# Kernel tuning notes

Measured on AMD Instinct MI355X. Metric: run time of the kernel, lower is better.

Reference implementation:

```python
import jax, jax.numpy as jnp
import numpy as np

SHAPE = (4096, 8192)


def setup_inputs() -> dict:
    key = jax.random.key(0)
    k1, k2 = jax.random.split(key)
    weights = jax.random.normal(k1, SHAPE, dtype=jnp.float32)
    mask_weights = jax.random.normal(k2, SHAPE, dtype=jnp.float32)
    return {
        "weights": weights,
        "mask_weights": mask_weights,
        "masking_percent_x100": 50,
    }


def reference(weights, mask_weights, masking_percent_x100):
    # Faithful to MaskingFunction.forward:
    #   k = int((1 - masking_percent) * N); zero the k SMALLEST mask_weights positions in weights.
    masking_percent = masking_percent_x100 / 100.0
    n = mask_weights.size  # static
    k = int((1.0 - masking_percent) * n)  # static Python int -> jit-compatible
    flat_mask = mask_weights.reshape(-1)
    # bottom-k == top-k of negated values
    _, bottomk_idx = jax.lax.top_k(-flat_mask, k)
    masked = weights.reshape(-1).at[bottomk_idx].set(0.0)
    return masked.reshape(weights.shape)
```

## Files before the change

### kernel.cpp

```cpp
#include <hip/hip_runtime.h>


#define NBINS 2048
#define CAP1 (1u << 22)
#define CAP2 65536u

__device__ unsigned int       g_hist1[NBINS];
__device__ unsigned int       g_hist2[NBINS];
__device__ unsigned int       g_count1;
__device__ unsigned int       g_count2;
__device__ unsigned int       g_cand_u[CAP1];
__device__ unsigned int       g_cand_i[CAP1];
__device__ unsigned long long g_cand2[CAP2];

static __device__ __forceinline__ unsigned int xf(unsigned int b) {
  return b ^ ((unsigned int)((int)b >> 31) | 0x80000000u);
}

static __device__ __forceinline__ long long compute_k(const int* mp, long long n) {
  long long m = (long long)(*mp);
  long long k = (n * (100 - m)) / 100;
  if (k < 0) k = 0;
  if (k > n) k = n;
  return k;
}

__global__ __launch_bounds__(256) void hist1_kernel(const unsigned int* __restrict__ mb,
                                                    long long n4, long long n) {
  __shared__ unsigned int sh[4 * NBINS];
  const int t = threadIdx.x;
  for (int i = t; i < 4 * NBINS; i += 256) sh[i] = 0;
  __syncthreads();
  unsigned int* h = &sh[(t >> 6) * NBINS];
  const uint4* mb4 = (const uint4*)mb;
  const long long stride = (long long)gridDim.x * 1024;
  long long i0 = (long long)blockIdx.x * 1024 + t;
  for (; i0 + 768 < n4; i0 += stride) {
    uint4 v0 = mb4[i0];
    uint4 v1 = mb4[i0 + 256];
    uint4 v2 = mb4[i0 + 512];
    uint4 v3 = mb4[i0 + 768];
    atomicAdd(&h[xf(v0.x) >> 21], 1u);
    atomicAdd(&h[xf(v0.y) >> 21], 1u);
    atomicAdd(&h[xf(v0.z) >> 21], 1u);
    atomicAdd(&h[xf(v0.w) >> 21], 1u);
    atomicAdd(&h[xf(v1.x) >> 21], 1u);
    atomicAdd(&h[xf(v1.y) >> 21], 1u);
    atomicAdd(&h[xf(v1.z) >> 21], 1u);
    atomicAdd(&h[xf(v1.w) >> 21], 1u);
    atomicAdd(&h[xf(v2.x) >> 21], 1u);
    atomicAdd(&h[xf(v2.y) >> 21], 1u);
    atomicAdd(&h[xf(v2.z) >> 21], 1u);
    atomicAdd(&h[xf(v2.w) >> 21], 1u);
    atomicAdd(&h[xf(v3.x) >> 21], 1u);
    atomicAdd(&h[xf(v3.y) >> 21], 1u);
    atomicAdd(&h[xf(v3.z) >> 21], 1u);
    atomicAdd(&h[xf(v3.w) >> 21], 1u);
  }
  for (int g = 0; g < 3; ++g) {
    long long i = i0 + (long long)g * 256;
    if (i < n4) {
      uint4 v = mb4[i];
      atomicAdd(&h[xf(v.x) >> 21], 1u);
      atomicAdd(&h[xf(v.y) >> 21], 1u);
      atomicAdd(&h[xf(v.z) >> 21], 1u);
      atomicAdd(&h[xf(v.w) >> 21], 1u);
    }
  }
  if (blockIdx.x == 0) {
    long long rs = n4 << 2;
    if ((long long)t < n - rs) atomicAdd(&h[xf(mb[rs + t]) >> 21], 1u);
  }
  __syncthreads();
  for (int i = t; i < NBINS; i += 256) {
    unsigned int s = sh[i] + sh[i + NBINS] + sh[i + 2 * NBINS] + sh[i + 3 * NBINS];
    if (s) atomicAdd(&g_hist1[i], s);
  }
}

static __device__ __forceinline__ void cand_add(unsigned int u, unsigned int idx) {
  unsigned int s = atomicAdd(&g_count1, 1u);
  if (s < CAP1) { g_cand_u[s] = u; g_cand_i[s] = idx; }
  atomicAdd(&g_hist2[(u >> 10) & (NBINS - 1)], 1u);
}

static __device__ __forceinline__ void proc4(long long i, uint4 mv, float4 wv,
                                             float4* __restrict__ o4, long long b1) {
  unsigned int u0 = xf(mv.x), u1 = xf(mv.y), u2 = xf(mv.z), u3 = xf(mv.w);
  float4 o;
  o.x = ((long long)(u0 >> 21) < b1) ? 0.0f : wv.x;
  o.y = ((long long)(u1 >> 21) < b1) ? 0.0f : wv.y;
  o.z = ((long long)(u2 >> 21) < b1) ? 0.0f : wv.z;
  o.w = ((long long)(u3 >> 21) < b1) ? 0.0f : wv.w;
  o4[i] = o;
  long long base = i << 2;
  if ((long long)(u0 >> 21) == b1) cand_add(u0, (unsigned int)(base + 0));
  if ((long long)(u1 >> 21) == b1) cand_add(u1, (unsigned int)(base + 1));
  if ((long long)(u2 >> 21) == b1) cand_add(u2, (unsigned int)(base + 2));
  if ((long long)(u3 >> 21) == b1) cand_add(u3, (unsigned int)(base + 3));
}

__global__ __launch_bounds__(256) void pass2_kernel(const unsigned int* __restrict__ mb,
                                                    const float* __restrict__ w,
                                                    float* __restrict__ out,
                                                    const int* __restrict__ mp,
                                                    long long n4, long long n) {
  __shared__ unsigned long long tsum[256];
  __shared__ long long s_b1;
  const int t = threadIdx.x;
  if (t == 0) s_b1 = -1;
  __syncthreads();
  const unsigned long long k = (unsigned long long)compute_k(mp, n);
  if (k != 0) {
    unsigned int local[8];
    unsigned long long s = 0;
#pragma unroll
    for (int j = 0; j < 8; j++) { local[j] = g_hist1[t * 8 + j]; s += local[j]; }
    tsum[t] = s;
    __syncthreads();
    for (int off = 1; off < 256; off <<= 1) {
      unsigned long long v = (t >= off) ? tsum[t - off] : 0ull;
      __syncthreads();
      tsum[t] += v;
      __syncthreads();
    }
    unsigned long long incl = tsum[t], excl = incl - s;
    if (excl < k && k <= incl) {
      unsigned long long cum = excl;
#pragma unroll
      for (int j = 0; j < 8; j++) {
        if (cum + local[j] >= k) { s_b1 = t * 8 + j; break; }
        cum += local[j];
      }
    }
  }
  __syncthreads();
  const long long b1 = s_b1;

  const uint4*  mb4 = (const uint4*)mb;
  const float4* w4  = (const float4*)w;
  float4*       o4  = (float4*)out;
  const long long stride = (long long)gridDim.x * 512;
  long long i0 = (long long)blockIdx.x * 512 + t;
  for (; i0 + 256 < n4; i0 += stride) {
    uint4  mv0 = mb4[i0];
    uint4  mv1 = mb4[i0 + 256];
    float4 wv0 = w4[i0];
    float4 wv1 = w4[i0 + 256];
    proc4(i0, mv0, wv0, o4, b1);
    proc4(i0 + 256, mv1, wv1, o4, b1);
  }
  if (i0 < n4) {
    uint4  mv = mb4[i0];
    float4 wv = w4[i0];
    proc4(i0, mv, wv, o4, b1);
  }
  if (blockIdx.x == 0) {
    long long rs = n4 << 2;
    long long i = rs + t;
    if (i < n) {
      unsigned int u = xf(mb[i]);
      out[i] = ((long long)(u >> 21) < b1) ? 0.0f : w[i];
      if ((long long)(u >> 21) == b1) cand_add(u, (unsigned int)i);
    }
  }
}

__global__ __launch_bounds__(256) void finalize_kernel(const int* __restrict__ mp,
                                                       float* __restrict__ out,
                                                       long long n) {
  __shared__ unsigned long long tsum[256];
  __shared__ long long s_b2;
  __shared__ unsigned long long s_rem1, s_rem2, s_kstar;
  const int t = threadIdx.x;
  const unsigned long long k = (unsigned long long)compute_k(mp, n);
  if (k != 0) {
    if (t == 0) s_kstar = 0;
    {
      unsigned int local[8];
      unsigned long long s = 0;
#pragma unroll
      for (int j = 0; j < 8; j++) { local[j] = g_hist1[t * 8 + j]; s += local[j]; }
      tsum[t] = s;
      __syncthreads();
      for (int off = 1; off < 256; off <<= 1) {
        unsigned long long v = (t >= off) ? tsum[t - off] : 0ull;
        __syncthreads();
        tsum[t] += v;
        __syncthreads();
      }
      unsigned long long incl = tsum[t], excl = incl - s;
      if (excl < k && k <= incl) {
        unsigned long long cum = excl;
#pragma unroll
        for (int j = 0; j < 8; j++) {
          if (cum + local[j] >= k) { s_rem1 = k - cum; break; }
          cum += local[j];
        }
      }
      __syncthreads();
    }
    {
      unsigned long long k2 = s_rem1;
      __syncthreads();
      unsigned int local[8];
      unsigned long long s = 0;
#pragma unroll
      for (int j = 0; j < 8; j++) { local[j] = g_hist2[t * 8 + j]; s += local[j]; }
      tsum[t] = s;
      __syncthreads();
      for (int off = 1; off < 256; off <<= 1) {
        unsigned long long v = (t >= off) ? tsum[t - off] : 0ull;
        __syncthreads();
        tsum[t] += v;
        __syncthreads();
      }
      unsigned long long incl = tsum[t], excl = incl - s;
      if (excl < k2 && k2 <= incl) {
        unsigned long long cum = excl;
#pragma unroll
        for (int j = 0; j < 8; j++) {
          if (cum + local[j] >= k2) { s_b2 = t * 8 + j; s_rem2 = k2 - cum; break; }
          cum += local[j];
        }
      }
      __syncthreads();
    }
    const unsigned int b2 = (unsigned int)s_b2;
    const unsigned int C = (g_count1 < CAP1) ? g_count1 : CAP1;
    for (unsigned int i = t; i < C; i += 256) {
      unsigned int u = g_cand_u[i];
      if (((u >> 10) & (NBINS - 1)) == b2) {
        unsigned int slot = atomicAdd(&g_count2, 1u);
        if (slot < CAP2) g_cand2[slot] = ((unsigned long long)u << 32) | (unsigned long long)g_cand_i[i];
      }
    }
    __threadfence();
    __syncthreads();
    unsigned int c2 = atomicAdd(&g_count2, 0u);
    const unsigned int C2 = (c2 < CAP2) ? c2 : CAP2;
    const unsigned long long rem2 = s_rem2;
    for (unsigned int i = t; i < C2; i += 256) {
      unsigned long long key = g_cand2[i];
      unsigned long long cnt = 0;
      for (unsigned int j = 0; j < C2; j++) cnt += (g_cand2[j] < key) ? 1ull : 0ull;
      if (cnt + 1 == rem2) s_kstar = key + 1;
    }
    __syncthreads();
    const unsigned long long kstar = s_kstar;
    for (unsigned int i = t; i < C; i += 256) {
      unsigned int idx = g_cand_i[i];
      unsigned long long key = ((unsigned long long)g_cand_u[i] << 32) | (unsigned long long)idx;
      if (key < kstar) out[idx] = 0.0f;
    }
  }
  __syncthreads();
  for (int i = t; i < NBINS; i += 256) { g_hist1[i] = 0; g_hist2[i] = 0; }
  if (t == 0) { g_count1 = 0; g_count2 = 0; }
}

extern "C" void kernel_launch(void* const* d_in, const int* in_sizes, int n_in,
                              void* d_out, int out_size, void* d_ws, size_t ws_size,
                              hipStream_t stream) {
  const float*        w  = (const float*)d_in[0];
  const unsigned int* mb = (const unsigned int*)d_in[1];
  const int*          mp = (const int*)d_in[2];
  float* out = (float*)d_out;
  const long long n  = (long long)in_sizes[0];
  const long long n4 = n >> 2;

  long long g1 = (n4 + 1023) / 1024;
  if (g1 < 1) g1 = 1;
  if (g1 > 1024) g1 = 1024;
  long long g2 = (n4 + 511) / 512;
  if (g2 < 1) g2 = 1;
  if (g2 > 2048) g2 = 2048;

  hist1_kernel<<<(int)g1, 256, 0, stream>>>(mb, n4, n);
  pass2_kernel<<<(int)g2, 256, 0, stream>>>(mb, w, out, mp, n4, n);
  finalize_kernel<<<1, 256, 0, stream>>>(mp, out, n);
}
```

Before: 354.1 us.

## Fuse finalize into pass2 via last-block pattern, add nontemporal accesses

The separate finalize kernel is removed. Its work now runs inside pass2 in whichever block finishes last, detected through an atomic done counter, and pass2 hands over the remaining-k value it already computes so the first histogram scan is not repeated. Weight loads and output stores use nontemporal builtins to reduce cache pollution. The histogram kernel drops from four to two shared sub-histograms per block and its grid cap is raised. This saves a kernel launch and a redundant scan, in exchange for a grid-wide atomic handoff and more shared-memory atomic contention per sub-histogram.

```diff
diff --git a/kernel.cpp b/kernel.cpp
--- a/kernel.cpp
+++ b/kernel.cpp
@@ -4,11 +4,15 @@
 #define NBINS 2048
 #define CAP1 (1u << 22)
 #define CAP2 65536u
+
+typedef float        vfloat4 __attribute__((ext_vector_type(4)));
+typedef unsigned int vuint4  __attribute__((ext_vector_type(4)));
 
 __device__ unsigned int       g_hist1[NBINS];
 __device__ unsigned int       g_hist2[NBINS];
 __device__ unsigned int       g_count1;
 __device__ unsigned int       g_count2;
+__device__ unsigned int       g_done;
 __device__ unsigned int       g_cand_u[CAP1];
 __device__ unsigned int       g_cand_i[CAP1];
 __device__ unsigned long long g_cand2[CAP2];
@@ -27,19 +31,19 @@
 
 __global__ __launch_bounds__(256) void hist1_kernel(const unsigned int* __restrict__ mb,
                                                     long long n4, long long n) {
-  __shared__ unsigned int sh[4 * NBINS];
+  __shared__ unsigned int sh[2 * NBINS];
   const int t = threadIdx.x;
-  for (int i = t; i < 4 * NBINS; i += 256) sh[i] = 0;
-  __syncthreads();
-  unsigned int* h = &sh[(t >> 6) * NBINS];
-  const uint4* mb4 = (const uint4*)mb;
+  for (int i = t; i < 2 * NBINS; i += 256) sh[i] = 0;
+  __syncthreads();
+  unsigned int* h = &sh[(t >> 7) * NBINS];
+  const vuint4* mb4 = (const vuint4*)mb;
   const long long stride = (long long)gridDim.x * 1024;
   long long i0 = (long long)blockIdx.x * 1024 + t;
   for (; i0 + 768 < n4; i0 += stride) {
-    uint4 v0 = mb4[i0];
-    uint4 v1 = mb4[i0 + 256];
-    uint4 v2 = mb4[i0 + 512];
-    uint4 v3 = mb4[i0 + 768];
+    vuint4 v0 = mb4[i0];
+    vuint4 v1 = mb4[i0 + 256];
+    vuint4 v2 = mb4[i0 + 512];
+    vuint4 v3 = mb4[i0 + 768];
     atomicAdd(&h[xf(v0.x) >> 21], 1u);
     atomicAdd(&h[xf(v0.y) >> 21], 1u);
     atomicAdd(&h[xf(v0.z) >> 21], 1u);
@@ -60,7 +64,7 @@
   for (int g = 0; g < 3; ++g) {
     long long i = i0 + (long long)g * 256;
     if (i < n4) {
-      uint4 v = mb4[i];
+      vuint4 v = mb4[i];
       atomicAdd(&h[xf(v.x) >> 21], 1u);
       atomicAdd(&h[xf(v.y) >> 21], 1u);
       atomicAdd(&h[xf(v.z) >> 21], 1u);
@@ -73,7 +77,7 @@
   }
   __syncthreads();
   for (int i = t; i < NBINS; i += 256) {
-    unsigned int s = sh[i] + sh[i + NBINS] + sh[i + 2 * NBINS] + sh[i + 3 * NBINS];
+    unsigned int s = sh[i] + sh[i + NBINS];
     if (s) atomicAdd(&g_hist1[i], s);
   }
 }
@@ -84,15 +88,15 @@
   atomicAdd(&g_hist2[(u >> 10) & (NBINS - 1)], 1u);
 }
 
-static __device__ __forceinline__ void proc4(long long i, uint4 mv, float4 wv,
-                                             float4* __restrict__ o4, long long b1) {
+static __device__ __forceinline__ void proc4(long long i, vuint4 mv, vfloat4 wv,
+                                             vfloat4* __restrict__ o4, long long b1) {
   unsigned int u0 = xf(mv.x), u1 = xf(mv.y), u2 = xf(mv.z), u3 = xf(mv.w);
-  float4 o;
+  vfloat4 o;
   o.x = ((long long)(u0 >> 21) < b1) ? 0.0f : wv.x;
   o.y = ((long long)(u1 >> 21) < b1) ? 0.0f : wv.y;
   o.z = ((long long)(u2 >> 21) < b1) ? 0.0f : wv.z;
   o.w = ((long long)(u3 >> 21) < b1) ? 0.0f : wv.w;
-  o4[i] = o;
+  __builtin_nontemporal_store(o, &o4[i]);
   long long base = i << 2;
   if ((long long)(u0 >> 21) == b1) cand_add(u0, (unsigned int)(base + 0));
   if ((long long)(u1 >> 21) == b1) cand_add(u1, (unsigned int)(base + 1));
@@ -107,8 +111,10 @@
                                                     long long n4, long long n) {
   __shared__ unsigned long long tsum[256];
   __shared__ long long s_b1;
+  __shared__ unsigned long long s_rem1;
+  __shared__ unsigned int s_last;
   const int t = threadIdx.x;
-  if (t == 0) s_b1 = -1;
+  if (t == 0) { s_b1 = -1; s_rem1 = 0; }
   __syncthreads();
   const unsigned long long k = (unsigned long long)compute_k(mp, n);
   if (k != 0) {
@@ -129,7 +135,7 @@
       unsigned long long cum = excl;
 #pragma unroll
       for (int j = 0; j < 8; j++) {
-        if (cum + local[j] >= k) { s_b1 = t * 8 + j; break; }
+        if (cum + local[j] >= k) { s_b1 = t * 8 + j; s_rem1 = k - cum; break; }
         cum += local[j];
       }
     }
@@ -137,22 +143,22 @@
   __syncthreads();
   const long long b1 = s_b1;
 
-  const uint4*  mb4 = (const uint4*)mb;
-  const float4* w4  = (const float4*)w;
-  float4*       o4  = (float4*)out;
+  const vuint4*  mb4 = (const vuint4*)mb;
+  const vfloat4* w4  = (const vfloat4*)w;
+  vfloat4*       o4  = (vfloat4*)out;
   const long long stride = (long long)gridDim.x * 512;
   long long i0 = (long long)blockIdx.x * 512 + t;
   for (; i0 + 256 < n4; i0 += stride) {
-    uint4  mv0 = mb4[i0];
-    uint4  mv1 = mb4[i0 + 256];
-    float4 wv0 = w4[i0];
-    float4 wv1 = w4[i0 + 256];
+    vuint4  mv0 = mb4[i0];
+    vuint4  mv1 = mb4[i0 + 256];
+    vfloat4 wv0 = __builtin_nontemporal_load(&w4[i0]);
+    vfloat4 wv1 = __builtin_nontemporal_load(&w4[i0 + 256]);
     proc4(i0, mv0, wv0, o4, b1);
     proc4(i0 + 256, mv1, wv1, o4, b1);
   }
   if (i0 < n4) {
-    uint4  mv = mb4[i0];
-    float4 wv = w4[i0];
+    vuint4  mv = mb4[i0];
+    vfloat4 wv = __builtin_nontemporal_load(&w4[i0]);
     proc4(i0, mv, wv, o4, b1);
   }
   if (blockIdx.x == 0) {
@@ -164,45 +170,20 @@
       if ((long long)(u >> 21) == b1) cand_add(u, (unsigned int)i);
     }
   }
-}
-
-__global__ __launch_bounds__(256) void finalize_kernel(const int* __restrict__ mp,
-                                                       float* __restrict__ out,
-                                                       long long n) {
-  __shared__ unsigned long long tsum[256];
-  __shared__ long long s_b2;
-  __shared__ unsigned long long s_rem1, s_rem2, s_kstar;
-  const int t = threadIdx.x;
-  const unsigned long long k = (unsigned long long)compute_k(mp, n);
+
+  __threadfence();
+  __syncthreads();
+  if (t == 0) s_last = (atomicAdd(&g_done, 1u) == (unsigned int)gridDim.x - 1u) ? 1u : 0u;
+  __syncthreads();
+  if (!s_last) return;
+  __threadfence();
+
   if (k != 0) {
+    __shared__ long long s_b2;
+    __shared__ unsigned long long s_rem2, s_kstar;
     if (t == 0) s_kstar = 0;
     {
-      unsigned int local[8];
-      unsigned long long s = 0;
-#pragma unroll
-      for (int j = 0; j < 8; j++) { local[j] = g_hist1[t * 8 + j]; s += local[j]; }
-      tsum[t] = s;
-      __syncthreads();
-      for (int off = 1; off < 256; off <<= 1) {
-        unsigned long long v = (t >= off) ? tsum[t - off] : 0ull;
-        __syncthreads();
-        tsum[t] += v;
-        __syncthreads();
-      }
-      unsigned long long incl = tsum[t], excl = incl - s;
-      if (excl < k && k <= incl) {
-        unsigned long long cum = excl;
-#pragma unroll
-        for (int j = 0; j < 8; j++) {
-          if (cum + local[j] >= k) { s_rem1 = k - cum; break; }
-          cum += local[j];
-        }
-      }
-      __syncthreads();
-    }
-    {
-      unsigned long long k2 = s_rem1;
-      __syncthreads();
+      const unsigned long long k2 = s_rem1;
       unsigned int local[8];
       unsigned long long s = 0;
 #pragma unroll
@@ -235,7 +216,6 @@
         if (slot < CAP2) g_cand2[slot] = ((unsigned long long)u << 32) | (unsigned long long)g_cand_i[i];
       }
     }
-    __threadfence();
     __syncthreads();
     unsigned int c2 = atomicAdd(&g_count2, 0u);
     const unsigned int C2 = (c2 < CAP2) ? c2 : CAP2;
@@ -253,10 +233,10 @@
       unsigned long long key = ((unsigned long long)g_cand_u[i] << 32) | (unsigned long long)idx;
       if (key < kstar) out[idx] = 0.0f;
     }
-  }
-  __syncthreads();
+    __syncthreads();
+  }
   for (int i = t; i < NBINS; i += 256) { g_hist1[i] = 0; g_hist2[i] = 0; }
-  if (t == 0) { g_count1 = 0; g_count2 = 0; }
+  if (t == 0) { g_count1 = 0; g_count2 = 0; __threadfence(); g_done = 0; }
 }
 
 extern "C" void kernel_launch(void* const* d_in, const int* in_sizes, int n_in,
@@ -271,12 +251,11 @@
 
   long long g1 = (n4 + 1023) / 1024;
   if (g1 < 1) g1 = 1;
-  if (g1 > 1024) g1 = 1024;
+  if (g1 > 2048) g1 = 2048;
   long long g2 = (n4 + 511) / 512;
   if (g2 < 1) g2 = 1;
   if (g2 > 2048) g2 = 2048;
 
   hist1_kernel<<<(int)g1, 256, 0, stream>>>(mb, n4, n);
   pass2_kernel<<<(int)g2, 256, 0, stream>>>(mb, w, out, mp, n4, n);
-  finalize_kernel<<<1, 256, 0, stream>>>(mp, out, n);
-}
+}
```

Result: slower. 714.3 us (+101.7%).
